# Kernel optimization log

Hardware: AMD Instinct MI355X
Metric: run time of the kernel (lower is better)

## Reference

```python
import jax, jax.numpy as jnp
import numpy as np

N_NODES = 10000
N_EDGES = 640000
D = 128            # node_dims == edge_dims
HID = 2 * D        # ff hidden
EPS = 1e-6


def _layernorm(x, g, b):
    mu = jnp.mean(x, axis=-1, keepdims=True)
    var = jnp.var(x, axis=-1, keepdims=True)
    return (x - mu) * jax.lax.rsqrt(var + EPS) * g + b


def setup_inputs() -> dict:
    key = jax.random.key(0)
    ks = jax.random.split(key, 16)
    def lin(k, fan_in, fan_out):
        lim = 1.0 / np.sqrt(fan_in)
        kw, kb = jax.random.split(k)
        W = jax.random.uniform(kw, (fan_in, fan_out), jnp.float32, -lim, lim)
        b = jax.random.uniform(kb, (fan_out,), jnp.float32, -lim, lim)
        return W, b
    x = jax.random.normal(ks[0], (N_NODES, D), jnp.float32)
    edge_index = jax.random.randint(ks[1], (2, N_EDGES), 0, N_NODES, jnp.int64)
    edge_attr = jax.random.normal(ks[2], (N_EDGES, D), jnp.float32)
    # message MLP: Linear(3D->D), ReLU, Linear(D->D), ReLU, Linear(D->D)
    W1, b1 = lin(ks[3], 3 * D, D)
    W2, b2 = lin(ks[4], D, D)
    W3, b3 = lin(ks[5], D, D)
    # feedforward: Linear(D->2D), ReLU, Linear(2D->D)
    F1, bf1 = lin(ks[6], D, HID)
    F2, bf2 = lin(ks[7], HID, D)
    g0 = jnp.ones((D,), jnp.float32); be0 = jnp.zeros((D,), jnp.float32)
    g1 = jnp.ones((D,), jnp.float32); be1 = jnp.zeros((D,), jnp.float32)
    return {"x": x, "edge_index": edge_index, "edge_attr": edge_attr,
            "W1": W1, "b1": b1, "W2": W2, "b2": b2, "W3": W3, "b3": b3,
            "F1": F1, "bf1": bf1, "F2": F2, "bf2": bf2,
            "g0": g0, "be0": be0, "g1": g1, "be1": be1}


def reference(x, edge_index, edge_attr, W1, b1, W2, b2, W3, b3,
              F1, bf1, F2, bf2, g0, be0, g1, be1):
    src = edge_index[0]  # j
    dst = edge_index[1]  # i
    # message: cat([h_V_i, edge_attr, h_V_j]) -> MLP  (E x 3D gather)
    m = jnp.concatenate([x[dst], edge_attr, x[src]], axis=-1)
    m = jax.nn.relu(m @ W1 + b1)
    m = jax.nn.relu(m @ W2 + b2)
    m = m @ W3 + b3  # [E, D]
    # scatter-mean over destination nodes
    sums = jax.ops.segment_sum(m, dst, num_segments=N_NODES)
    cnt = jax.ops.segment_sum(jnp.ones((N_EDGES,), m.dtype), dst, num_segments=N_NODES)
    dh = sums / jnp.maximum(cnt, 1.0)[:, None]
    # residual + norm (dropout is identity at inference)
    h = _layernorm(x + dh, g0, be0)
    # pointwise feedforward
    ff = jax.nn.relu(h @ F1 + bf1) @ F2 + bf2
    return _layernorm(h + ff, g1, be1)
```

## Files before the change

kernel.cpp:

```cpp
#include <hip/hip_runtime.h>


#define NE 640000
#define NN 10000
#define DD 128
#define HIDN 256
#define EPSF 1e-6f

typedef __attribute__((ext_vector_type(8))) short short8;
typedef __attribute__((ext_vector_type(4))) float f32x4;

__device__ __forceinline__ unsigned short f2bf(float f) {
    union { float f; unsigned int u; } v; v.f = f;
    unsigned int r = v.u + 0x7FFFu + ((v.u >> 16) & 1u);
    return (unsigned short)(r >> 16);
}
__device__ __forceinline__ float bf2f(unsigned short h) {
    union { unsigned int u; float f; } v; v.u = ((unsigned int)h) << 16;
    return v.f;
}

__global__ void prep_weights(const float* __restrict__ W1,
                             const float* __restrict__ W2,
                             const float* __restrict__ W3,
                             unsigned short* __restrict__ WT)
{
    int g = blockIdx.x * 256 + threadIdx.x;
    int layer = g >> 14, r = g & 16383;
    int n = r >> 7, k = r & 127;
    const float* W = (layer == 0) ? (W1 + 128 * DD) : (layer == 1 ? W2 : W3);
    WT[layer * 16384 + n * 128 + ((((k >> 3) ^ (n & 7)) << 3) | (k & 7))] =
        f2bf(W[k * DD + n]);
}

__global__ __launch_bounds__(256, 2)
void pq_kernel(const float* __restrict__ x, const float* __restrict__ W1,
               const float* __restrict__ b1,
               unsigned short* __restrict__ Pb, unsigned short* __restrict__ Qb)
{
    __shared__ float sXT[128 * 68];
    __shared__ float sB[32 * 128];
    const int t = threadIdx.x;
    const int nb = blockIdx.x * 64;
    const int r0 = (t >> 4) << 2, c0 = (t & 15) << 3;

#pragma unroll
    for (int p = 0; p < 8; ++p) {
        int f = t + p * 256;
        int row = f >> 5, c4 = (f & 31) << 2;
        int node = nb + row; if (node >= NN) node = NN - 1;
        float4 v = *(const float4*)(x + (long)node * DD + c4);
        sXT[(c4 + 0) * 68 + row] = v.x;
        sXT[(c4 + 1) * 68 + row] = v.y;
        sXT[(c4 + 2) * 68 + row] = v.z;
        sXT[(c4 + 3) * 68 + row] = v.w;
    }

    for (int pass = 0; pass < 2; ++pass) {
        const float* W = W1 + (pass == 0 ? 0 : 256 * DD);
        float acc[4][8];
#pragma unroll
        for (int i = 0; i < 4; ++i)
#pragma unroll
            for (int j = 0; j < 8; ++j) acc[i][j] = 0.f;

        for (int kc = 0; kc < 4; ++kc) {
            __syncthreads();
#pragma unroll
            for (int p = 0; p < 4; ++p) {
                int f = t + p * 256;
                int kr = f >> 5, col = (f & 31) << 2;
                *(float4*)(sB + kr * 128 + col) =
                    *(const float4*)(W + (long)(kc * 32 + kr) * DD + col);
            }
            __syncthreads();
#pragma unroll 4
            for (int k = 0; k < 32; ++k) {
                float4 a  = *(const float4*)(sXT + (kc * 32 + k) * 68 + r0);
                float4 bl = *(const float4*)(sB + k * 128 + c0);
                float4 bh = *(const float4*)(sB + k * 128 + c0 + 4);
                float av[4] = {a.x, a.y, a.z, a.w};
                float bv[8] = {bl.x, bl.y, bl.z, bl.w, bh.x, bh.y, bh.z, bh.w};
#pragma unroll
                for (int i = 0; i < 4; ++i)
#pragma unroll
                    for (int j = 0; j < 8; ++j)
                        acc[i][j] = fmaf(av[i], bv[j], acc[i][j]);
            }
        }
        unsigned short* Out = (pass == 0) ? Pb : Qb;
#pragma unroll
        for (int i = 0; i < 4; ++i) {
            int node = nb + r0 + i;
            if (node < NN) {
                unsigned short tmp[8];
#pragma unroll
                for (int j = 0; j < 8; ++j) {
                    float v = acc[i][j] + (pass == 0 ? b1[c0 + j] : 0.f);
                    tmp[j] = f2bf(v);
                }
                *(uint4*)(Out + (long)node * 128 + c0) = *(uint4*)tmp;
            }
        }
    }
}

__global__ void hist_kernel(const int* __restrict__ ei, int* __restrict__ cursor)
{
    int e = blockIdx.x * 256 + threadIdx.x;
    if (e < NE) atomicAdd(cursor + ei[(long)NE + e], 1);
}

__global__ __launch_bounds__(256)
void scan_kernel(int* __restrict__ cursor, float* __restrict__ cnt)
{
    __shared__ int sp[256];
    const int t = threadIdx.x;
    const int base = t * 40;
    int v[40], loc[40];
    int s = 0;
#pragma unroll
    for (int i = 0; i < 40; ++i) {
        int n = base + i;
        v[i] = (n < NN) ? cursor[n] : 0;
        loc[i] = s; s += v[i];
    }
    sp[t] = s;
    __syncthreads();
    for (int off = 1; off < 256; off <<= 1) {
        int x = 0;
        if (t >= off) x = sp[t - off];
        __syncthreads();
        sp[t] += x;
        __syncthreads();
    }
    int excl = sp[t] - s;
#pragma unroll
    for (int i = 0; i < 40; ++i) {
        int n = base + i;
        if (n < NN) {
            cursor[n] = excl + loc[i];
            cnt[n] = (float)v[i];
        }
    }
}

__global__ void scatter_kernel(const int* __restrict__ ei,
                               int* __restrict__ cursor, int* __restrict__ perm)
{
    int e = blockIdx.x * 256 + threadIdx.x;
    if (e < NE) {
        int d = ei[(long)NE + e];
        int p = atomicAdd(cursor + d, 1);
        perm[p] = e;
    }
}

__device__ __forceinline__ const short8* frag(const unsigned short* buf,
                                              int row, int kc, int q)
{
    int g = (kc * 4 + q) ^ (row & 7);
    return (const short8*)(buf + row * 128 + g * 8);
}

__global__ __launch_bounds__(256, 2)
void edge_mfma(const float* __restrict__ ea, const int* __restrict__ ei,
               const int* __restrict__ perm,
               const unsigned short* __restrict__ WT,
               const unsigned short* __restrict__ Pb,
               const unsigned short* __restrict__ Qb,
               const float* __restrict__ b2, const float* __restrict__ b3,
               float* __restrict__ sums)
{
    __shared__ __align__(16) char smem[66560];
    unsigned short* sA = (unsigned short*)smem;
    unsigned short* sW = (unsigned short*)(smem + 32768);
    float*          sM = (float*)smem;
    int*            sE   = (int*)(smem + 65536);
    int*            sDst = (int*)(smem + 66048);

    const int t = threadIdx.x;
    const int wave = t >> 6, lane = t & 63;
    const int ln = lane & 15, q = lane >> 4;
    const int r0 = wave * 32;
    const long pbase = (long)blockIdx.x * 128;

    if (t < 128) {
        int e = perm[pbase + t];
        sE[t] = e;
        sDst[t] = ei[(long)NE + e];
    }
    {
        const uint4* src = (const uint4*)WT;
        uint4* dst = (uint4*)sW;
#pragma unroll
        for (int p = 0; p < 8; ++p) dst[t + p * 256] = src[t + p * 256];
    }
    __syncthreads();

    int drow[8], srow[8];
#pragma unroll
    for (int rt = 0; rt < 2; ++rt)
#pragma unroll
        for (int rg = 0; rg < 4; ++rg) {
            int row = r0 + rt * 16 + q * 4 + rg;
            drow[rt * 4 + rg] = sDst[row];
            srow[rt * 4 + rg] = ei[sE[row]];
        }

#pragma unroll
    for (int p = 0; p < 16; ++p) {
        int f = t + p * 256;
        int row = f >> 5, c4 = (f & 31) << 2;
        float4 v = *(const float4*)(ea + (long)sE[row] * DD + c4);
        uint2 pk;
        pk.x = (unsigned)f2bf(v.x) | ((unsigned)f2bf(v.y) << 16);
        pk.y = (unsigned)f2bf(v.z) | ((unsigned)f2bf(v.w) << 16);
        int addr = row * 128 + ((((c4 >> 3) ^ (row & 7)) << 3) | (c4 & 7));
        *(uint2*)(sA + addr) = pk;
    }
    __syncthreads();

    f32x4 acc[2][8];

#pragma unroll
    for (int rt = 0; rt < 2; ++rt)
#pragma unroll
        for (int ct = 0; ct < 8; ++ct) acc[rt][ct] = (f32x4)(0.f);
#pragma unroll
    for (int kc = 0; kc < 4; ++kc) {
        short8 a0 = *frag(sA, r0 + ln,      kc, q);
        short8 a1 = *frag(sA, r0 + 16 + ln, kc, q);
#pragma unroll
        for (int ct = 0; ct < 8; ++ct) {
            short8 b = *frag(sW, ct * 16 + ln, kc, q);
            acc[0][ct] = __builtin_amdgcn_mfma_f32_16x16x32_bf16(a0, b, acc[0][ct], 0, 0, 0);
            acc[1][ct] = __builtin_amdgcn_mfma_f32_16x16x32_bf16(a1, b, acc[1][ct], 0, 0, 0);
        }
    }
    __syncthreads();
    {
        const uint4* src = (const uint4*)(WT + 16384);
        uint4* dst = (uint4*)sW;
#pragma unroll
        for (int p = 0; p < 8; ++p) dst[t + p * 256] = src[t + p * 256];
    }
#pragma unroll
    for (int rt = 0; rt < 2; ++rt)
#pragma unroll
        for (int rg = 0; rg < 4; ++rg) {
            int row = r0 + rt * 16 + q * 4 + rg;
            long dof = (long)drow[rt * 4 + rg] * DD;
            long sof = (long)srow[rt * 4 + rg] * DD;
#pragma unroll
            for (int ct = 0; ct < 8; ++ct) {
                int col = ct * 16 + ln;
                float v = acc[rt][ct][rg] + bf2f(Pb[dof + col]) + bf2f(Qb[sof + col]);
                v = fmaxf(v, 0.f);
                sA[row * 128 + ((((col >> 3) ^ (row & 7)) << 3) | (col & 7))] = f2bf(v);
            }
        }
    __syncthreads();

#pragma unroll
    for (int rt = 0; rt < 2; ++rt)
#pragma unroll
        for (int ct = 0; ct < 8; ++ct) acc[rt][ct] = (f32x4)(0.f);
#pragma unroll
    for (int kc = 0; kc < 4; ++kc) {
        short8 a0 = *frag(sA, r0 + ln,      kc, q);
        short8 a1 = *frag(sA, r0 + 16 + ln, kc, q);
#pragma unroll
        for (int ct = 0; ct < 8; ++ct) {
            short8 b = *frag(sW, ct * 16 + ln, kc, q);
            acc[0][ct] = __builtin_amdgcn_mfma_f32_16x16x32_bf16(a0, b, acc[0][ct], 0, 0, 0);
            acc[1][ct] = __builtin_amdgcn_mfma_f32_16x16x32_bf16(a1, b, acc[1][ct], 0, 0, 0);
        }
    }
    __syncthreads();
    {
        const uint4* src = (const uint4*)(WT + 2 * 16384);
        uint4* dst = (uint4*)sW;
#pragma unroll
        for (int p = 0; p < 8; ++p) dst[t + p * 256] = src[t + p * 256];
    }
    float bv2[8];
#pragma unroll
    for (int ct = 0; ct < 8; ++ct) bv2[ct] = b2[ct * 16 + ln];
#pragma unroll
    for (int rt = 0; rt < 2; ++rt)
#pragma unroll
        for (int rg = 0; rg < 4; ++rg) {
            int row = r0 + rt * 16 + q * 4 + rg;
#pragma unroll
            for (int ct = 0; ct < 8; ++ct) {
                int col = ct * 16 + ln;
                float v = fmaxf(acc[rt][ct][rg] + bv2[ct], 0.f);
                sA[row * 128 + ((((col >> 3) ^ (row & 7)) << 3) | (col & 7))] = f2bf(v);
            }
        }
    __syncthreads();

#pragma unroll
    for (int rt = 0; rt < 2; ++rt)
#pragma unroll
        for (int ct = 0; ct < 8; ++ct) acc[rt][ct] = (f32x4)(0.f);
#pragma unroll
    for (int kc = 0; kc < 4; ++kc) {
        short8 a0 = *frag(sA, r0 + ln,      kc, q);
        short8 a1 = *frag(sA, r0 + 16 + ln, kc, q);
#pragma unroll
        for (int ct = 0; ct < 8; ++ct) {
            short8 b = *frag(sW, ct * 16 + ln, kc, q);
            acc[0][ct] = __builtin_amdgcn_mfma_f32_16x16x32_bf16(a0, b, acc[0][ct], 0, 0, 0);
            acc[1][ct] = __builtin_amdgcn_mfma_f32_16x16x32_bf16(a1, b, acc[1][ct], 0, 0, 0);
        }
    }

    float bv3[8];
#pragma unroll
    for (int ct = 0; ct < 8; ++ct) bv3[ct] = b3[ct * 16 + ln];
    __syncthreads();
#pragma unroll
    for (int rt = 0; rt < 2; ++rt)
#pragma unroll
        for (int rg = 0; rg < 4; ++rg) {
            int row = r0 + rt * 16 + q * 4 + rg;
#pragma unroll
            for (int ct = 0; ct < 8; ++ct)
                sM[row * 128 + ct * 16 + ln] = acc[rt][ct][rg] + bv3[ct];
        }
    __syncthreads();

    {
        const int c = t & 127, h = t >> 7;
        const int rb = h * 64;
        float a = 0.f;
        int cur = sDst[rb];
#pragma unroll 8
        for (int r = rb; r < rb + 64; ++r) {
            int d = sDst[r];
            if (d != cur) {
                atomicAdd(sums + (long)cur * DD + c, a);
                a = 0.f; cur = d;
            }
            a += sM[r * 128 + c];
        }
        atomicAdd(sums + (long)cur * DD + c, a);
    }
}

__global__ __launch_bounds__(256)
void node_fused(const float* __restrict__ x,
                const float* __restrict__ sums, const float* __restrict__ cnt,
                const float* __restrict__ F1, const float* __restrict__ bf1,
                const float* __restrict__ F2, const float* __restrict__ bf2,
                const float* __restrict__ g0, const float* __restrict__ be0,
                const float* __restrict__ g1, const float* __restrict__ be1,
                float* __restrict__ out)
{
    constexpr int NPB = 8;
    __shared__ float sh[NPB][DD];
    __shared__ float shid[NPB][HIDN];
    __shared__ float sz[NPB][DD];

    const int t = threadIdx.x;
    const int wave = t >> 6, lane = t & 63;
    const int half = lane >> 5, l2 = lane & 31;
    const int nl = wave * 2 + half;
    const int node = blockIdx.x * NPB + nl;
    const long base = (long)node * DD;

    float inv = 1.0f / fmaxf(cnt[node], 1.0f);
    float y[4], s = 0.f, ss = 0.f;
#pragma unroll
    for (int e = 0; e < 4; ++e) {
        int c = l2 + 32 * e;
        y[e] = x[base + c] + sums[base + c] * inv;
        s += y[e]; ss += y[e] * y[e];
    }
#pragma unroll
    for (int off = 16; off > 0; off >>= 1) {
        s += __shfl_down(s, off, 32); ss += __shfl_down(ss, off, 32);
    }
    s = __shfl(s, 0, 32); ss = __shfl(ss, 0, 32);
    float mean = s * (1.0f / DD);
    float var  = ss * (1.0f / DD) - mean * mean;
    float rstd = rsqrtf(var + EPSF);
#pragma unroll
    for (int e = 0; e < 4; ++e) {
        int c = l2 + 32 * e;
        sh[nl][c] = (y[e] - mean) * rstd * g0[c] + be0[c];
    }
    __syncthreads();

    float hacc[NPB];
    float bb = bf1[t];
#pragma unroll
    for (int v = 0; v < NPB; ++v) hacc[v] = bb;
    for (int k = 0; k < DD; ++k) {
        float wv = F1[(long)k * HIDN + t];
#pragma unroll
        for (int v = 0; v < NPB; ++v) hacc[v] = fmaf(sh[v][k], wv, hacc[v]);
    }
#pragma unroll
    for (int v = 0; v < NPB; ++v) shid[v][t] = fmaxf(hacc[v], 0.f);
    __syncthreads();

    const int col = t & (DD - 1);
    const int grp = (t >> 7) * 4;
    float o[4];
#pragma unroll
    for (int v = 0; v < 4; ++v) o[v] = bf2[col];
    for (int k = 0; k < HIDN; ++k) {
        float wv = F2[(long)k * DD + col];
#pragma unroll
        for (int v = 0; v < 4; ++v) o[v] = fmaf(shid[grp + v][k], wv, o[v]);
    }
#pragma unroll
    for (int v = 0; v < 4; ++v) sz[grp + v][col] = sh[grp + v][col] + o[v];
    __syncthreads();

    float z[4]; s = 0.f; ss = 0.f;
#pragma unroll
    for (int e = 0; e < 4; ++e) {
        int c = l2 + 32 * e;
        z[e] = sz[nl][c]; s += z[e]; ss += z[e] * z[e];
    }
#pragma unroll
    for (int off = 16; off > 0; off >>= 1) {
        s += __shfl_down(s, off, 32); ss += __shfl_down(ss, off, 32);
    }
    s = __shfl(s, 0, 32); ss = __shfl(ss, 0, 32);
    mean = s * (1.0f / DD);
    var  = ss * (1.0f / DD) - mean * mean;
    rstd = rsqrtf(var + EPSF);
#pragma unroll
    for (int e = 0; e < 4; ++e) {
        int c = l2 + 32 * e;
        out[base + c] = (z[e] - mean) * rstd * g1[c] + be1[c];
    }
}

extern "C" void kernel_launch(void* const* d_in, const int* in_sizes, int n_in,
                              void* d_out, int out_size, void* d_ws, size_t ws_size,
                              hipStream_t stream)
{
    const float* x   = (const float*)d_in[0];
    const int*   ei  = (const int*)  d_in[1];
    const float* ea  = (const float*)d_in[2];
    const float* W1  = (const float*)d_in[3];
    const float* b1  = (const float*)d_in[4];
    const float* W2  = (const float*)d_in[5];
    const float* b2  = (const float*)d_in[6];
    const float* W3  = (const float*)d_in[7];
    const float* b3  = (const float*)d_in[8];
    const float* F1  = (const float*)d_in[9];
    const float* bf1 = (const float*)d_in[10];
    const float* F2  = (const float*)d_in[11];
    const float* bf2 = (const float*)d_in[12];
    const float* g0  = (const float*)d_in[13];
    const float* be0 = (const float*)d_in[14];
    const float* g1  = (const float*)d_in[15];
    const float* be1 = (const float*)d_in[16];
    float* out = (float*)d_out;

    char* ws = (char*)d_ws;
    float*          sums   = (float*)(ws);
    float*          cnt    = (float*)(ws + 5120000);
    unsigned short* WT     = (unsigned short*)(ws + 5160192);
    unsigned short* Pb     = (unsigned short*)(ws + 5258752);
    unsigned short* Qb     = (unsigned short*)(ws + 7818752);
    int*            cursor = (int*)(ws + 10378752);
    int*            perm   = (int*)(ws + 10418752);

    hipMemsetAsync(ws, 0, 5120000, stream);
    hipMemsetAsync(ws + 10378752, 0, 40000, stream);
    prep_weights<<<192, 256, 0, stream>>>(W1, W2, W3, WT);
    pq_kernel<<<(NN + 63) / 64, 256, 0, stream>>>(x, W1, b1, Pb, Qb);
    hist_kernel<<<NE / 256, 256, 0, stream>>>(ei, cursor);
    scan_kernel<<<1, 256, 0, stream>>>(cursor, cnt);
    scatter_kernel<<<NE / 256, 256, 0, stream>>>(ei, cursor, perm);
    edge_mfma<<<NE / 128, 256, 0, stream>>>(ea, ei, perm, WT, Pb, Qb,
                                            b2, b3, sums);
    node_fused<<<NN / 8, 256, 0, stream>>>(x, sums, cnt, F1, bf1, F2, bf2,
                                           g0, be0, g1, be1, out);
}
```

Baseline: 788.0 us.

## Shrink edge kernel LDS footprint to raise occupancy, stream weights from global

The weight tiles are no longer staged in shared memory; MFMA B fragments are read directly from global/L1 for all three GEMMs. The source-node Qb rows are gathered into the A buffer with coalesced vector loads and added in place, and the epilogue reduction is done in two 64-row halves with a padded stride of 132. Together these cut shared memory from about 66KB to about 35KB, which lets the launch bounds ask for 4 blocks per CU and drops several barriers. In exchange, every GEMM now pays global-memory latency for weight fragments and adds an extra reduction round.

Result: slower. 908.8 us (+15.3%).

```diff
diff --git a/kernel.cpp b/kernel.cpp
--- a/kernel.cpp
+++ b/kernel.cpp
@@ -163,7 +163,7 @@
     return (const short8*)(buf + row * 128 + g * 8);
 }
 
-__global__ __launch_bounds__(256, 2)
+__global__ __launch_bounds__(256, 4)
 void edge_mfma(const float* __restrict__ ea, const int* __restrict__ ei,
                const int* __restrict__ perm,
                const unsigned short* __restrict__ WT,
@@ -172,12 +172,12 @@
                const float* __restrict__ b2, const float* __restrict__ b3,
                float* __restrict__ sums)
 {
-    __shared__ __align__(16) char smem[66560];
-    unsigned short* sA = (unsigned short*)smem;
-    unsigned short* sW = (unsigned short*)(smem + 32768);
-    float*          sM = (float*)smem;
-    int*            sE   = (int*)(smem + 65536);
-    int*            sDst = (int*)(smem + 66048);
+    __shared__ __align__(16) char smem[1536 + 64 * 132 * 4];
+    int*            sE   = (int*)smem;
+    int*            sDst = (int*)(smem + 512);
+    int*            sSrc = (int*)(smem + 1024);
+    unsigned short* sA = (unsigned short*)(smem + 1536);
+    float*          sM = (float*)(smem + 1536);
 
     const int t = threadIdx.x;
     const int wave = t >> 6, lane = t & 63;
@@ -189,24 +189,9 @@
         int e = perm[pbase + t];
         sE[t] = e;
         sDst[t] = ei[(long)NE + e];
-    }
-    {
-        const uint4* src = (const uint4*)WT;
-        uint4* dst = (uint4*)sW;
-#pragma unroll
-        for (int p = 0; p < 8; ++p) dst[t + p * 256] = src[t + p * 256];
-    }
-    __syncthreads();
-
-    int drow[8], srow[8];
-#pragma unroll
-    for (int rt = 0; rt < 2; ++rt)
-#pragma unroll
-        for (int rg = 0; rg < 4; ++rg) {
-            int row = r0 + rt * 16 + q * 4 + rg;
-            drow[rt * 4 + rg] = sDst[row];
-            srow[rt * 4 + rg] = ei[sE[row]];
-        }
+        sSrc[t] = ei[e];
+    }
+    __syncthreads();
 
 #pragma unroll
     for (int p = 0; p < 16; ++p) {
@@ -233,34 +218,36 @@
         short8 a1 = *frag(sA, r0 + 16 + ln, kc, q);
 #pragma unroll
         for (int ct = 0; ct < 8; ++ct) {
-            short8 b = *frag(sW, ct * 16 + ln, kc, q);
+            short8 b = *frag(WT, ct * 16 + ln, kc, q);
             acc[0][ct] = __builtin_amdgcn_mfma_f32_16x16x32_bf16(a0, b, acc[0][ct], 0, 0, 0);
             acc[1][ct] = __builtin_amdgcn_mfma_f32_16x16x32_bf16(a1, b, acc[1][ct], 0, 0, 0);
         }
     }
     __syncthreads();
-    {
-        const uint4* src = (const uint4*)(WT + 16384);
-        uint4* dst = (uint4*)sW;
-#pragma unroll
-        for (int p = 0; p < 8; ++p) dst[t + p * 256] = src[t + p * 256];
-    }
+
+#pragma unroll
+    for (int p = 0; p < 8; ++p) {
+        int f = t + p * 256;
+        int row = f >> 4, g = f & 15;
+        uint4 v = *(const uint4*)(Qb + (long)sSrc[row] * DD + g * 8);
+        *(uint4*)(sA + row * 128 + ((g ^ (row & 7)) << 3)) = v;
+    }
+    __syncthreads();
+
 #pragma unroll
     for (int rt = 0; rt < 2; ++rt)
 #pragma unroll
         for (int rg = 0; rg < 4; ++rg) {
             int row = r0 + rt * 16 + q * 4 + rg;
-            long dof = (long)drow[rt * 4 + rg] * DD;
-            long sof = (long)srow[rt * 4 + rg] * DD;
+            long dof = (long)sDst[row] * DD;
 #pragma unroll
             for (int ct = 0; ct < 8; ++ct) {
                 int col = ct * 16 + ln;
-                float v = acc[rt][ct][rg] + bf2f(Pb[dof + col]) + bf2f(Qb[sof + col]);
-                v = fmaxf(v, 0.f);
-                sA[row * 128 + ((((col >> 3) ^ (row & 7)) << 3) | (col & 7))] = f2bf(v);
-            }
-        }
-    __syncthreads();
+                int slot = row * 128 + ((((col >> 3) ^ (row & 7)) << 3) | (col & 7));
+                float v = acc[rt][ct][rg] + bf2f(Pb[dof + col]) + bf2f(sA[slot]);
+                sA[slot] = f2bf(fmaxf(v, 0.f));
+            }
+        }
 
 #pragma unroll
     for (int rt = 0; rt < 2; ++rt)
@@ -272,18 +259,11 @@
         short8 a1 = *frag(sA, r0 + 16 + ln, kc, q);
 #pragma unroll
         for (int ct = 0; ct < 8; ++ct) {
-            short8 b = *frag(sW, ct * 16 + ln, kc, q);
+            short8 b = *frag(WT + 16384, ct * 16 + ln, kc, q);
             acc[0][ct] = __builtin_amdgcn_mfma_f32_16x16x32_bf16(a0, b, acc[0][ct], 0, 0, 0);
             acc[1][ct] = __builtin_amdgcn_mfma_f32_16x16x32_bf16(a1, b, acc[1][ct], 0, 0, 0);
         }
     }
-    __syncthreads();
-    {
-        const uint4* src = (const uint4*)(WT + 2 * 16384);
-        uint4* dst = (uint4*)sW;
-#pragma unroll
-        for (int p = 0; p < 8; ++p) dst[t + p * 256] = src[t + p * 256];
-    }
     float bv2[8];
 #pragma unroll
     for (int ct = 0; ct < 8; ++ct) bv2[ct] = b2[ct * 16 + ln];
@@ -295,11 +275,10 @@
 #pragma unroll
             for (int ct = 0; ct < 8; ++ct) {
                 int col = ct * 16 + ln;
-                float v = fmaxf(acc[rt][ct][rg] + bv2[ct], 0.f);
-                sA[row * 128 + ((((col >> 3) ^ (row & 7)) << 3) | (col & 7))] = f2bf(v);
-            }
-        }
-    __syncthreads();
+                int slot = row * 128 + ((((col >> 3) ^ (row & 7)) << 3) | (col & 7));
+                sA[slot] = f2bf(fmaxf(acc[rt][ct][rg] + bv2[ct], 0.f));
+            }
+        }
 
 #pragma unroll
     for (int rt = 0; rt < 2; ++rt)
@@ -311,40 +290,71 @@
         short8 a1 = *frag(sA, r0 + 16 + ln, kc, q);
 #pragma unroll
         for (int ct = 0; ct < 8; ++ct) {
-            short8 b = *frag(sW, ct * 16 + ln, kc, q);
+            short8 b = *frag(WT + 2 * 16384, ct * 16 + ln, kc, q);
             acc[0][ct] = __builtin_amdgcn_mfma_f32_16x16x32_bf16(a0, b, acc[0][ct], 0, 0, 0);
             acc[1][ct] = __builtin_amdgcn_mfma_f32_16x16x32_bf16(a1, b, acc[1][ct], 0, 0, 0);
         }
     }
+    __syncthreads();
 
     float bv3[8];
 #pragma unroll
     for (int ct = 0; ct < 8; ++ct) bv3[ct] = b3[ct * 16 + ln];
-    __syncthreads();
-#pragma unroll
-    for (int rt = 0; rt < 2; ++rt)
-#pragma unroll
-        for (int rg = 0; rg < 4; ++rg) {
-            int row = r0 + rt * 16 + q * 4 + rg;
-#pragma unroll
-            for (int ct = 0; ct < 8; ++ct)
-                sM[row * 128 + ct * 16 + ln] = acc[rt][ct][rg] + bv3[ct];
-        }
-    __syncthreads();
-
+
+    if (wave < 2) {
+#pragma unroll
+        for (int rt = 0; rt < 2; ++rt)
+#pragma unroll
+            for (int rg = 0; rg < 4; ++rg) {
+                int row = r0 + rt * 16 + q * 4 + rg;
+#pragma unroll
+                for (int ct = 0; ct < 8; ++ct)
+                    sM[row * 132 + ct * 16 + ln] = acc[rt][ct][rg] + bv3[ct];
+            }
+    }
+    __syncthreads();
     {
         const int c = t & 127, h = t >> 7;
-        const int rb = h * 64;
+        const int rb = h * 32;
         float a = 0.f;
         int cur = sDst[rb];
 #pragma unroll 8
-        for (int r = rb; r < rb + 64; ++r) {
+        for (int r = rb; r < rb + 32; ++r) {
             int d = sDst[r];
             if (d != cur) {
                 atomicAdd(sums + (long)cur * DD + c, a);
                 a = 0.f; cur = d;
             }
-            a += sM[r * 128 + c];
+            a += sM[r * 132 + c];
+        }
+        atomicAdd(sums + (long)cur * DD + c, a);
+    }
+    __syncthreads();
+    if (wave >= 2) {
+#pragma unroll
+        for (int rt = 0; rt < 2; ++rt)
+#pragma unroll
+            for (int rg = 0; rg < 4; ++rg) {
+                int row = r0 + rt * 16 + q * 4 + rg;
+#pragma unroll
+                for (int ct = 0; ct < 8; ++ct)
+                    sM[(row - 64) * 132 + ct * 16 + ln] = acc[rt][ct][rg] + bv3[ct];
+            }
+    }
+    __syncthreads();
+    {
+        const int c = t & 127, h = t >> 7;
+        const int rb = h * 32;
+        float a = 0.f;
+        int cur = sDst[64 + rb];
+#pragma unroll 8
+        for (int r = rb; r < rb + 32; ++r) {
+            int d = sDst[64 + r];
+            if (d != cur) {
+                atomicAdd(sums + (long)cur * DD + c, a);
+                a = 0.f; cur = d;
+            }
+            a += sM[r * 132 + c];
         }
         atomicAdd(sums + (long)cur * DD + c, a);
     }
```
